# Performance work log

Measured on AMD Instinct MI355X. Metric: run time of the kernel, lower is better.

The kernel has to match this reference:

```python
import jax, jax.numpy as jnp
import numpy as np

N_AGENTS, HIDDEN, MSG, KEY = 8192, 256, 128, 64

def _glorot(k, shape):
    fan_in, fan_out = shape[0], shape[1]
    lim = jnp.sqrt(6.0 / (fan_in + fan_out))
    return jax.random.uniform(k, shape, jnp.float32, -lim, lim)

def setup_inputs() -> dict:
    key = jax.random.key(0)
    ks = jax.random.split(key, 12)
    inp = {
        'h': jax.random.normal(ks[0], (N_AGENTS, HIDDEN), jnp.float32),
        'W_msg': _glorot(ks[1], (HIDDEN, MSG)), 'b_msg': jnp.zeros((MSG,), jnp.float32),
        'W_key': _glorot(ks[2], (HIDDEN, KEY)), 'b_key': jnp.zeros((KEY,), jnp.float32),
        'W_qry': _glorot(ks[3], (HIDDEN, KEY)), 'b_qry': jnp.zeros((KEY,), jnp.float32),
        # GRUCell: input (attended message, dim MSG) -> hidden; gates r,z,n
        'Wi_r': _glorot(ks[4], (MSG, HIDDEN)), 'bi_r': jnp.zeros((HIDDEN,), jnp.float32),
        'Wi_z': _glorot(ks[5], (MSG, HIDDEN)), 'bi_z': jnp.zeros((HIDDEN,), jnp.float32),
        'Wi_n': _glorot(ks[6], (MSG, HIDDEN)), 'bi_n': jnp.zeros((HIDDEN,), jnp.float32),
        'Wh_r': _glorot(ks[7], (HIDDEN, HIDDEN)),
        'Wh_z': _glorot(ks[8], (HIDDEN, HIDDEN)),
        'Wh_n': _glorot(ks[9], (HIDDEN, HIDDEN)), 'bh_n': jnp.zeros((HIDDEN,), jnp.float32),
    }
    return inp

def reference(h, W_msg, b_msg, W_key, b_key, W_qry, b_qry,
              Wi_r, bi_r, Wi_z, bi_z, Wi_n, bi_n, Wh_r, Wh_z, Wh_n, bh_n):
    n = h.shape[0]
    messages = h @ W_msg + b_msg            # [N, MSG]
    keys = h @ W_key + b_key                # [N, KEY]
    queries = h @ W_qry + b_qry             # [N, KEY]
    scale = jnp.sqrt(jnp.float32(keys.shape[-1]))
    scores = (queries @ keys.T) / scale     # [N, N]
    scores = jnp.clip(scores, -20.0, 20.0)
    self_mask = jnp.eye(n, dtype=scores.dtype)
    scores = jnp.where(self_mask > 0, -1e8, scores)
    attn_weights = jax.nn.softmax(scores, axis=-1)
    attended = attn_weights @ messages      # [N, MSG]
    # flax GRUCell: carry = h, inputs = attended
    r = jax.nn.sigmoid(attended @ Wi_r + bi_r + h @ Wh_r)
    z = jax.nn.sigmoid(attended @ Wi_z + bi_z + h @ Wh_z)
    cand = jnp.tanh(attended @ Wi_n + bi_n + r * (h @ Wh_n + bh_n))
    h_new = (1.0 - z) * cand + z * h
    return (h_new, attn_weights)
```

## Files before the change

### kernel.cpp

```cpp
#include <hip/hip_runtime.h>
#include <math.h>

#define N_AGENTS 8192
#define HIDDEN   256
#define MSG      128
#define KEYD     64
#define CSPLIT   4

#define OFF_WM_H   0
#define OFF_WM_L   32768
#define OFF_WK_H   65536
#define OFF_WK_L   81920
#define OFF_WQ_H   98304
#define OFF_WQ_L   114688
#define OFF_WIR_H  131072
#define OFF_WIR_L  163840
#define OFF_WIZ_H  196608
#define OFF_WIZ_L  229376
#define OFF_WIN_H  262144
#define OFF_WIN_L  294912
#define OFF_WHR_H  327680
#define OFF_WHR_L  393216
#define OFF_WHZ_H  458752
#define OFF_WHZ_L  524288
#define OFF_WHN_H  589824
#define OFF_WHN_L  655360
#define WT_TOTAL   720896

typedef __attribute__((ext_vector_type(8))) short short8_t;
typedef __attribute__((ext_vector_type(4))) short short4_t;
typedef __attribute__((ext_vector_type(4))) float float4_t;

__device__ __forceinline__ short f2bf(float x) {
    unsigned u = __float_as_uint(x);
    unsigned r = (u + 0x7fffu + ((u >> 16) & 1u)) >> 16;
    return (short)r;
}
__device__ __forceinline__ float bf2f(short b) {
    return __uint_as_float(((unsigned)(unsigned short)b) << 16);
}
__device__ __forceinline__ void split4(float4 v, short4_t* hi, short4_t* lo) {
    (*hi)[0] = f2bf(v.x); (*lo)[0] = f2bf(v.x - bf2f((*hi)[0]));
    (*hi)[1] = f2bf(v.y); (*lo)[1] = f2bf(v.y - bf2f((*hi)[1]));
    (*hi)[2] = f2bf(v.z); (*lo)[2] = f2bf(v.z - bf2f((*hi)[2]));
    (*hi)[3] = f2bf(v.w); (*lo)[3] = f2bf(v.w - bf2f((*hi)[3]));
}

__global__ __launch_bounds__(256) void prep_weights(
    const float* __restrict__ Wm, const float* __restrict__ Wk, const float* __restrict__ Wq,
    const float* __restrict__ Wir, const float* __restrict__ Wiz, const float* __restrict__ Win,
    const float* __restrict__ Whr, const float* __restrict__ Whz, const float* __restrict__ Whn,
    short* __restrict__ wT)
{
    int idx = blockIdx.x * 256 + threadIdx.x;
    const float* src; int K, lgC, local; size_t oh, ol;
    if (idx < 32768)        { src = Wm;  K = 256; lgC = 7; local = idx;          oh = OFF_WM_H;  ol = OFF_WM_L; }
    else if (idx < 49152)   { src = Wk;  K = 256; lgC = 6; local = idx - 32768;  oh = OFF_WK_H;  ol = OFF_WK_L; }
    else if (idx < 65536)   { src = Wq;  K = 256; lgC = 6; local = idx - 49152;  oh = OFF_WQ_H;  ol = OFF_WQ_L; }
    else if (idx < 98304)   { src = Wir; K = 128; lgC = 8; local = idx - 65536;  oh = OFF_WIR_H; ol = OFF_WIR_L; }
    else if (idx < 131072)  { src = Wiz; K = 128; lgC = 8; local = idx - 98304;  oh = OFF_WIZ_H; ol = OFF_WIZ_L; }
    else if (idx < 163840)  { src = Win; K = 128; lgC = 8; local = idx - 131072; oh = OFF_WIN_H; ol = OFF_WIN_L; }
    else if (idx < 229376)  { src = Whr; K = 256; lgC = 8; local = idx - 163840; oh = OFF_WHR_H; ol = OFF_WHR_L; }
    else if (idx < 294912)  { src = Whz; K = 256; lgC = 8; local = idx - 229376; oh = OFF_WHZ_H; ol = OFF_WHZ_L; }
    else if (idx < 360448)  { src = Whn; K = 256; lgC = 8; local = idx - 294912; oh = OFF_WHN_H; ol = OFF_WHN_L; }
    else return;
    int k = local >> lgC, c = local & ((1 << lgC) - 1);
    float v = src[local];
    short hi = f2bf(v);
    short lo = f2bf(v - bf2f(hi));
    wT[oh + (size_t)c * K + k] = hi;
    wT[ol + (size_t)c * K + k] = lo;
}

__global__ __launch_bounds__(256) void proj_mfma_kernel(
    const float* __restrict__ h, const short* __restrict__ wT,
    const float* __restrict__ bm, const float* __restrict__ bk, const float* __restrict__ bq,
    short* __restrict__ msgTb,
    short* __restrict__ qh, short* __restrict__ ql,
    short* __restrict__ kh, short* __restrict__ kl)
{
    __shared__ short hh[16][264], hl[16][264];
    int t = threadIdx.x;
    int wave = t >> 6, l = t & 63, quad = l >> 4, ln = l & 15;
    int i0 = blockIdx.x * 16;

#pragma unroll
    for (int p = 0; p < 4; p++) {
        int idx = t + p * 256;
        int r = idx >> 6, k4 = (idx & 63) * 4;
        float4 v = *(const float4*)&h[(size_t)(i0 + r) * HIDDEN + k4];
        short4_t hv, lv;
        split4(v, &hv, &lv);
        *(short4_t*)&hh[r][k4] = hv;
        *(short4_t*)&hl[r][k4] = lv;
    }
    __syncthreads();

    size_t base_h, base_l; int cb;
    if (wave < 2)      { base_h = OFF_WM_H; base_l = OFF_WM_L; cb = wave * 64; }
    else if (wave == 2){ base_h = OFF_WK_H; base_l = OFF_WK_L; cb = 0; }
    else               { base_h = OFF_WQ_H; base_l = OFF_WQ_L; cb = 0; }

    float4_t acc[4];
#pragma unroll
    for (int nt = 0; nt < 4; nt++) acc[nt] = (float4_t)0.f;

    for (int ch = 0; ch < 8; ch++) {
        short8_t a_h = *(short8_t*)&hh[ln][ch * 32 + quad * 8];
        short8_t a_l = *(short8_t*)&hl[ln][ch * 32 + quad * 8];
#pragma unroll
        for (int nt = 0; nt < 4; nt++) {
            int c = cb + nt * 16 + ln;
            const short* bp_h = wT + base_h + (size_t)c * 256 + ch * 32 + quad * 8;
            const short* bp_l = wT + base_l + (size_t)c * 256 + ch * 32 + quad * 8;
            short8_t b_h = *(const short8_t*)bp_h;
            short8_t b_l = *(const short8_t*)bp_l;
            acc[nt] = __builtin_amdgcn_mfma_f32_16x16x32_bf16(a_h, b_h, acc[nt], 0, 0, 0);
            acc[nt] = __builtin_amdgcn_mfma_f32_16x16x32_bf16(a_h, b_l, acc[nt], 0, 0, 0);
            acc[nt] = __builtin_amdgcn_mfma_f32_16x16x32_bf16(a_l, b_h, acc[nt], 0, 0, 0);
        }
    }

    if (wave < 2) {
#pragma unroll
        for (int nt = 0; nt < 4; nt++) {
            int col = cb + nt * 16 + ln;
            float b = bm[col];
            short4_t o;
#pragma unroll
            for (int reg = 0; reg < 4; reg++) o[reg] = f2bf(acc[nt][reg] + b);
            *(short4_t*)&msgTb[(size_t)col * N_AGENTS + i0 + quad * 4] = o;
        }
    } else {
        short* dh = (wave == 2) ? kh : qh;
        short* dl = (wave == 2) ? kl : ql;
        const float* bias = (wave == 2) ? bk : bq;
#pragma unroll
        for (int nt = 0; nt < 4; nt++) {
            int col = nt * 16 + ln;
            float b = bias[col];
#pragma unroll
            for (int reg = 0; reg < 4; reg++) {
                int row = i0 + quad * 4 + reg;
                float v = acc[nt][reg] + b;
                short hi = f2bf(v);
                short lo = f2bf(v - bf2f(hi));
                dh[(size_t)row * KEYD + col] = hi;
                dl[(size_t)row * KEYD + col] = lo;
            }
        }
    }
}

__global__ __launch_bounds__(256) void rowsum_kernel(
    const short* __restrict__ qh, const short* __restrict__ ql,
    const short* __restrict__ kh, const short* __restrict__ kl,
    float* __restrict__ rowsum)
{
    int t = threadIdx.x;
    int wave = t >> 6, l = t & 63;
    int quad = l >> 4, ln = l & 15;
    int i0 = blockIdx.y * 64;
    int j0 = blockIdx.x * 256 + wave * 64;

    short8_t ah[4][2], al[4][2];
#pragma unroll
    for (int r = 0; r < 4; r++)
#pragma unroll
        for (int ch = 0; ch < 2; ch++) {
            size_t off = (size_t)(i0 + r * 16 + ln) * KEYD + ch * 32 + quad * 8;
            ah[r][ch] = *(const short8_t*)(qh + off);
            al[r][ch] = *(const short8_t*)(ql + off);
        }

    float4_t acc[4][4];
#pragma unroll
    for (int r = 0; r < 4; r++)
#pragma unroll
        for (int c = 0; c < 4; c++) acc[r][c] = (float4_t)0.f;

#pragma unroll
    for (int c = 0; c < 4; c++) {
        int coln = j0 + c * 16 + ln;
#pragma unroll
        for (int ch = 0; ch < 2; ch++) {
            size_t off = (size_t)coln * KEYD + ch * 32 + quad * 8;
            short8_t bh = *(const short8_t*)(kh + off);
            short8_t bl = *(const short8_t*)(kl + off);
#pragma unroll
            for (int r = 0; r < 4; r++) {
                acc[r][c] = __builtin_amdgcn_mfma_f32_16x16x32_bf16(ah[r][ch], bh, acc[r][c], 0, 0, 0);
                acc[r][c] = __builtin_amdgcn_mfma_f32_16x16x32_bf16(ah[r][ch], bl, acc[r][c], 0, 0, 0);
                acc[r][c] = __builtin_amdgcn_mfma_f32_16x16x32_bf16(al[r][ch], bh, acc[r][c], 0, 0, 0);
            }
        }
    }

    float prow[4][4];
#pragma unroll
    for (int r = 0; r < 4; r++)
#pragma unroll
        for (int reg = 0; reg < 4; reg++) {
            int gi = i0 + r * 16 + quad * 4 + reg;
            float sum = 0.f;
#pragma unroll
            for (int c = 0; c < 4; c++) {
                float s = acc[r][c][reg] * 0.125f;
                s = fminf(fmaxf(s, -20.f), 20.f);
                int gj = j0 + c * 16 + ln;
                float p = (gi == gj) ? 0.f : __expf(s);
                sum += p;
            }
            prow[r][reg] = sum;
        }

#pragma unroll
    for (int off = 1; off < 16; off <<= 1)
#pragma unroll
        for (int r = 0; r < 4; r++)
#pragma unroll
            for (int reg = 0; reg < 4; reg++)
                prow[r][reg] += __shfl_xor(prow[r][reg], off);

    if (ln == 0) {
#pragma unroll
        for (int r = 0; r < 4; r++)
#pragma unroll
            for (int reg = 0; reg < 4; reg++)
                atomicAdd(&rowsum[i0 + r * 16 + quad * 4 + reg], prow[r][reg]);
    }
}

__global__ __launch_bounds__(256) void attend_fused_kernel(
    const short* __restrict__ qh, const short* __restrict__ ql,
    const short* __restrict__ kh, const short* __restrict__ kl,
    const short* __restrict__ msgTb, const float* __restrict__ rowsum,
    float* __restrict__ P, float* __restrict__ att_part)
{
    const int JB = 128;
    const int STR = JB + 8;
    __shared__ short A_lds[64][STR];
    __shared__ short B_lds[MSG][STR];
    __shared__ float inv_s[64];

    int t = threadIdx.x;
    int wave = t >> 6, l = t & 63;
    int quad = l >> 4, ln = l & 15;
    int i0 = blockIdx.y * 64;
    int kbase = blockIdx.x * (N_AGENTS / CSPLIT);

    if (t < 64) inv_s[t] = 1.0f / rowsum[i0 + t];

    short8_t ah[4][2], al[4][2];
#pragma unroll
    for (int r = 0; r < 4; r++)
#pragma unroll
        for (int ch = 0; ch < 2; ch++) {
            size_t off = (size_t)(i0 + r * 16 + ln) * KEYD + ch * 32 + quad * 8;
            ah[r][ch] = *(const short8_t*)(qh + off);
            al[r][ch] = *(const short8_t*)(ql + off);
        }

    float4_t accm[8];
#pragma unroll
    for (int c = 0; c < 8; c++) accm[c] = (float4_t)0.f;

    __syncthreads();

    for (int jt = 0; jt < N_AGENTS / CSPLIT; jt += JB) {
        int kpos = kbase + jt;

        float4_t acc[4][2];
#pragma unroll
        for (int r = 0; r < 4; r++)
#pragma unroll
            for (int c2 = 0; c2 < 2; c2++) acc[r][c2] = (float4_t)0.f;

#pragma unroll
        for (int c2 = 0; c2 < 2; c2++) {
            int coln = kpos + wave * 32 + c2 * 16 + ln;
#pragma unroll
            for (int ch = 0; ch < 2; ch++) {
                size_t off = (size_t)coln * KEYD + ch * 32 + quad * 8;
                short8_t bh = *(const short8_t*)(kh + off);
                short8_t bl = *(const short8_t*)(kl + off);
#pragma unroll
                for (int r = 0; r < 4; r++) {
                    acc[r][c2] = __builtin_amdgcn_mfma_f32_16x16x32_bf16(ah[r][ch], bh, acc[r][c2], 0, 0, 0);
                    acc[r][c2] = __builtin_amdgcn_mfma_f32_16x16x32_bf16(ah[r][ch], bl, acc[r][c2], 0, 0, 0);
                    acc[r][c2] = __builtin_amdgcn_mfma_f32_16x16x32_bf16(al[r][ch], bh, acc[r][c2], 0, 0, 0);
                }
            }
        }

        __syncthreads();

        short8_t bst[8];
#pragma unroll
        for (int p = 0; p < 8; p++) {
            int idx = t + p * 256;
            int c = idx >> 4, kk = (idx & 15) * 8;
            bst[p] = *(const short8_t*)(msgTb + (size_t)c * N_AGENTS + kpos + kk);
        }

        float pv[4][4][2];
#pragma unroll
        for (int r = 0; r < 4; r++)
#pragma unroll
            for (int reg = 0; reg < 4; reg++) {
                int row = r * 16 + quad * 4 + reg;
                int gi = i0 + row;
                float iv = inv_s[row];
#pragma unroll
                for (int c2 = 0; c2 < 2; c2++) {
                    int col = wave * 32 + c2 * 16 + ln;
                    int gj = kpos + col;
                    float s = acc[r][c2][reg] * 0.125f;
                    s = fminf(fmaxf(s, -20.f), 20.f);
                    float p = (gi == gj) ? 0.f : __expf(s) * iv;
                    pv[r][reg][c2] = p;
                    A_lds[row][col] = f2bf(p);
                }
            }

#pragma unroll
        for (int p = 0; p < 8; p++) {
            int idx = t + p * 256;
            int c = idx >> 4, kk = (idx & 15) * 8;
            *(short8_t*)&B_lds[c][kk] = bst[p];
        }

        __syncthreads();

#pragma unroll
        for (int r = 0; r < 4; r++)
#pragma unroll
            for (int reg = 0; reg < 4; reg++) {
                int gi = i0 + r * 16 + quad * 4 + reg;
#pragma unroll
                for (int c2 = 0; c2 < 2; c2++) {
                    int gj = kpos + wave * 32 + c2 * 16 + ln;
                    __builtin_nontemporal_store(pv[r][reg][c2], &P[(size_t)gi * N_AGENTS + gj]);
                }
            }

#pragma unroll
        for (int kc = 0; kc < 4; kc++) {
            short8_t a = *(short8_t*)&A_lds[wave * 16 + ln][kc * 32 + quad * 8];
#pragma unroll
            for (int c = 0; c < 8; c++) {
                short8_t b = *(short8_t*)&B_lds[c * 16 + ln][kc * 32 + quad * 8];
                accm[c] = __builtin_amdgcn_mfma_f32_16x16x32_bf16(a, b, accm[c], 0, 0, 0);
            }
        }
    }

    float* ap = att_part + (size_t)blockIdx.x * N_AGENTS * MSG;
#pragma unroll
    for (int c = 0; c < 8; c++)
#pragma unroll
        for (int reg = 0; reg < 4; reg++) {
            int row = i0 + wave * 16 + quad * 4 + reg;
            int col = c * 16 + ln;
            ap[(size_t)row * MSG + col] = accm[c][reg];
        }
}

__global__ __launch_bounds__(256) void gru_mfma_kernel(
    const float* __restrict__ att_part, const float* __restrict__ h,
    const short* __restrict__ wT,
    const float* __restrict__ bir, const float* __restrict__ biz,
    const float* __restrict__ bin, const float* __restrict__ bhn,
    float* __restrict__ hnew)
{
    __shared__ short ath[16][136], atl[16][136];
    __shared__ short hh[16][264], hl[16][264];
    int t = threadIdx.x;
    int wave = t >> 6, l = t & 63, quad = l >> 4, ln = l & 15;
    int i0 = blockIdx.x * 16;
    int cb = wave * 64;

#pragma unroll
    for (int p = 0; p < 2; p++) {
        int idx = t + p * 256;
        int r = idx >> 5, c4 = (idx & 31) * 4;
        size_t off = (size_t)(i0 + r) * MSG + c4;
        float4 v = *(const float4*)&att_part[off];
#pragma unroll
        for (int s = 1; s < CSPLIT; s++) {
            float4 w = *(const float4*)&att_part[(size_t)s * N_AGENTS * MSG + off];
            v.x += w.x; v.y += w.y; v.z += w.z; v.w += w.w;
        }
        short4_t hv, lv;
        split4(v, &hv, &lv);
        *(short4_t*)&ath[r][c4] = hv;
        *(short4_t*)&atl[r][c4] = lv;
    }
#pragma unroll
    for (int p = 0; p < 4; p++) {
        int idx = t + p * 256;
        int r = idx >> 6, k4 = (idx & 63) * 4;
        float4 v = *(const float4*)&h[(size_t)(i0 + r) * HIDDEN + k4];
        short4_t hv, lv;
        split4(v, &hv, &lv);
        *(short4_t*)&hh[r][k4] = hv;
        *(short4_t*)&hl[r][k4] = lv;
    }
    __syncthreads();

    float4_t ar[4], az[4], an[4], hn[4];
#pragma unroll
    for (int nt = 0; nt < 4; nt++) {
        ar[nt] = (float4_t)0.f; az[nt] = (float4_t)0.f;
        an[nt] = (float4_t)0.f; hn[nt] = (float4_t)0.f;
    }

#define MFMA3(ACC, AH, AL, BH, BL)                                              \
    ACC = __builtin_amdgcn_mfma_f32_16x16x32_bf16(AH, BH, ACC, 0, 0, 0);        \
    ACC = __builtin_amdgcn_mfma_f32_16x16x32_bf16(AH, BL, ACC, 0, 0, 0);        \
    ACC = __builtin_amdgcn_mfma_f32_16x16x32_bf16(AL, BH, ACC, 0, 0, 0);

    for (int ch = 0; ch < 4; ch++) {
        short8_t a_h = *(short8_t*)&ath[ln][ch * 32 + quad * 8];
        short8_t a_l = *(short8_t*)&atl[ln][ch * 32 + quad * 8];
#pragma unroll
        for (int nt = 0; nt < 4; nt++) {
            size_t cw = (size_t)(cb + nt * 16 + ln) * 128 + ch * 32 + quad * 8;
            short8_t brh = *(const short8_t*)(wT + OFF_WIR_H + cw);
            short8_t brl = *(const short8_t*)(wT + OFF_WIR_L + cw);
            MFMA3(ar[nt], a_h, a_l, brh, brl);
            short8_t bzh = *(const short8_t*)(wT + OFF_WIZ_H + cw);
            short8_t bzl = *(const short8_t*)(wT + OFF_WIZ_L + cw);
            MFMA3(az[nt], a_h, a_l, bzh, bzl);
            short8_t bnh = *(const short8_t*)(wT + OFF_WIN_H + cw);
            short8_t bnl = *(const short8_t*)(wT + OFF_WIN_L + cw);
            MFMA3(an[nt], a_h, a_l, bnh, bnl);
        }
    }

    for (int ch = 0; ch < 8; ch++) {
        short8_t a_h = *(short8_t*)&hh[ln][ch * 32 + quad * 8];
        short8_t a_l = *(short8_t*)&hl[ln][ch * 32 + quad * 8];
#pragma unroll
        for (int nt = 0; nt < 4; nt++) {
            size_t cw = (size_t)(cb + nt * 16 + ln) * 256 + ch * 32 + quad * 8;
            short8_t brh = *(const short8_t*)(wT + OFF_WHR_H + cw);
            short8_t brl = *(const short8_t*)(wT + OFF_WHR_L + cw);
            MFMA3(ar[nt], a_h, a_l, brh, brl);
            short8_t bzh = *(const short8_t*)(wT + OFF_WHZ_H + cw);
            short8_t bzl = *(const short8_t*)(wT + OFF_WHZ_L + cw);
            MFMA3(az[nt], a_h, a_l, bzh, bzl);
            short8_t bnh = *(const short8_t*)(wT + OFF_WHN_H + cw);
            short8_t bnl = *(const short8_t*)(wT + OFF_WHN_L + cw);
            MFMA3(hn[nt], a_h, a_l, bnh, bnl);
        }
    }
#undef MFMA3

#pragma unroll
    for (int nt = 0; nt < 4; nt++) {
        int col = cb + nt * 16 + ln;
        float br = bir[col], bz = biz[col], bn = bin[col], bh_ = bhn[col];
#pragma unroll
        for (int reg = 0; reg < 4; reg++) {
            int row = i0 + quad * 4 + reg;
            float hv = h[(size_t)row * HIDDEN + col];
            float rr = 1.f / (1.f + __expf(-(ar[nt][reg] + br)));
            float zz = 1.f / (1.f + __expf(-(az[nt][reg] + bz)));
            float cand = tanhf(an[nt][reg] + bn + rr * (hn[nt][reg] + bh_));
            hnew[(size_t)row * HIDDEN + col] = (1.f - zz) * cand + zz * hv;
        }
    }
}

extern "C" void kernel_launch(void* const* d_in, const int* in_sizes, int n_in,
                              void* d_out, int out_size, void* d_ws, size_t ws_size,
                              hipStream_t stream)
{
    const float* h     = (const float*)d_in[0];
    const float* W_msg = (const float*)d_in[1];
    const float* b_msg = (const float*)d_in[2];
    const float* W_key = (const float*)d_in[3];
    const float* b_key = (const float*)d_in[4];
    const float* W_qry = (const float*)d_in[5];
    const float* b_qry = (const float*)d_in[6];
    const float* Wi_r  = (const float*)d_in[7];
    const float* bi_r  = (const float*)d_in[8];
    const float* Wi_z  = (const float*)d_in[9];
    const float* bi_z  = (const float*)d_in[10];
    const float* Wi_n  = (const float*)d_in[11];
    const float* bi_n  = (const float*)d_in[12];
    const float* Wh_r  = (const float*)d_in[13];
    const float* Wh_z  = (const float*)d_in[14];
    const float* Wh_n  = (const float*)d_in[15];
    const float* bh_n  = (const float*)d_in[16];

    float* out  = (float*)d_out;
    float* hnew = out;
    float* P    = out + (size_t)N_AGENTS * HIDDEN;

    float* ws       = (float*)d_ws;
    float* rowsum   = ws;
    float* att_part = ws + N_AGENTS;
    short* sbase    = (short*)(att_part + (size_t)CSPLIT * N_AGENTS * MSG);
    short* msgTb    = sbase;
    short* qh       = msgTb + (size_t)MSG * N_AGENTS;
    short* ql       = qh + (size_t)N_AGENTS * KEYD;
    short* kh       = ql + (size_t)N_AGENTS * KEYD;
    short* kl       = kh + (size_t)N_AGENTS * KEYD;
    short* wT       = kl + (size_t)N_AGENTS * KEYD;

    hipMemsetAsync(rowsum, 0, (size_t)N_AGENTS * sizeof(float), stream);

    prep_weights<<<1408, 256, 0, stream>>>(W_msg, W_key, W_qry, Wi_r, Wi_z, Wi_n,
                                           Wh_r, Wh_z, Wh_n, wT);

    proj_mfma_kernel<<<N_AGENTS / 16, 256, 0, stream>>>(h, wT, b_msg, b_key, b_qry,
                                                        msgTb, qh, ql, kh, kl);

    rowsum_kernel<<<dim3(N_AGENTS / 256, N_AGENTS / 64), 256, 0, stream>>>(qh, ql, kh, kl, rowsum);

    attend_fused_kernel<<<dim3(CSPLIT, N_AGENTS / 64), 256, 0, stream>>>(qh, ql, kh, kl,
                                                                         msgTb, rowsum, P, att_part);

    gru_mfma_kernel<<<N_AGENTS / 16, 256, 0, stream>>>(att_part, h, wT, bi_r, bi_z, bi_n, bh_n, hnew);
}
```

Measured before the change: 595.8 us.

## Software-pipeline attend kernel with double-buffered LDS and replace rowsum atomics

The attention kernel now processes 64-column key tiles with double-buffered LDS. The next tile's key fragments and message slices are prefetched into registers, and its QK^T MFMAs are issued while the current tile's PV MFMAs run, so a barrier is removed per step. Rowsum atomics and the memset are replaced by per-block partial sums that are reduced in the attend kernel prologue. Launch bounds request 2 blocks per SIMD. These changes add register pressure and a strided partial-sum read.

```diff
diff --git a/kernel.cpp b/kernel.cpp
--- a/kernel.cpp
+++ b/kernel.cpp
@@ -6,6 +6,7 @@
 #define MSG      128
 #define KEYD     64
 #define CSPLIT   4
+#define NSTEP    (N_AGENTS / CSPLIT / 64)
 
 #define OFF_WM_H   0
 #define OFF_WM_L   32768
@@ -111,10 +112,8 @@
 #pragma unroll
         for (int nt = 0; nt < 4; nt++) {
             int c = cb + nt * 16 + ln;
-            const short* bp_h = wT + base_h + (size_t)c * 256 + ch * 32 + quad * 8;
-            const short* bp_l = wT + base_l + (size_t)c * 256 + ch * 32 + quad * 8;
-            short8_t b_h = *(const short8_t*)bp_h;
-            short8_t b_l = *(const short8_t*)bp_l;
+            short8_t b_h = *(const short8_t*)(wT + base_h + (size_t)c * 256 + ch * 32 + quad * 8);
+            short8_t b_l = *(const short8_t*)(wT + base_l + (size_t)c * 256 + ch * 32 + quad * 8);
             acc[nt] = __builtin_amdgcn_mfma_f32_16x16x32_bf16(a_h, b_h, acc[nt], 0, 0, 0);
             acc[nt] = __builtin_amdgcn_mfma_f32_16x16x32_bf16(a_h, b_l, acc[nt], 0, 0, 0);
             acc[nt] = __builtin_amdgcn_mfma_f32_16x16x32_bf16(a_l, b_h, acc[nt], 0, 0, 0);
@@ -155,7 +154,7 @@
 __global__ __launch_bounds__(256) void rowsum_kernel(
     const short* __restrict__ qh, const short* __restrict__ ql,
     const short* __restrict__ kh, const short* __restrict__ kl,
-    float* __restrict__ rowsum)
+    float* __restrict__ rowsum_part)
 {
     int t = threadIdx.x;
     int wave = t >> 6, l = t & 63;
@@ -223,24 +222,23 @@
                 prow[r][reg] += __shfl_xor(prow[r][reg], off);
 
     if (ln == 0) {
+        int pidx = blockIdx.x * 4 + wave;
 #pragma unroll
         for (int r = 0; r < 4; r++)
 #pragma unroll
             for (int reg = 0; reg < 4; reg++)
-                atomicAdd(&rowsum[i0 + r * 16 + quad * 4 + reg], prow[r][reg]);
-    }
-}
-
-__global__ __launch_bounds__(256) void attend_fused_kernel(
+                rowsum_part[(size_t)(i0 + r * 16 + quad * 4 + reg) * 128 + pidx] = prow[r][reg];
+    }
+}
+
+__global__ __launch_bounds__(256, 2) void attend_fused_kernel(
     const short* __restrict__ qh, const short* __restrict__ ql,
     const short* __restrict__ kh, const short* __restrict__ kl,
-    const short* __restrict__ msgTb, const float* __restrict__ rowsum,
+    const short* __restrict__ msgTb, const float* __restrict__ rowsum_part,
     float* __restrict__ P, float* __restrict__ att_part)
 {
-    const int JB = 128;
-    const int STR = JB + 8;
-    __shared__ short A_lds[64][STR];
-    __shared__ short B_lds[MSG][STR];
+    __shared__ short A_lds[2][64][72];
+    __shared__ short B_lds[2][128][72];
     __shared__ float inv_s[64];
 
     int t = threadIdx.x;
@@ -249,7 +247,16 @@
     int i0 = blockIdx.y * 64;
     int kbase = blockIdx.x * (N_AGENTS / CSPLIT);
 
-    if (t < 64) inv_s[t] = 1.0f / rowsum[i0 + t];
+    if (t < 64) {
+        const float* rp = rowsum_part + (size_t)(i0 + t) * 128;
+        float s = 0.f;
+#pragma unroll
+        for (int p = 0; p < 32; p++) {
+            float4 v = *(const float4*)(rp + p * 4);
+            s += v.x + v.y + v.z + v.w;
+        }
+        inv_s[t] = 1.0f / s;
+    }
 
     short8_t ah[4][2], al[4][2];
 #pragma unroll
@@ -265,69 +272,71 @@
 #pragma unroll
     for (int c = 0; c < 8; c++) accm[c] = (float4_t)0.f;
 
+    const int colL = wave * 16 + ln;
+
+    short8_t kfh[2], kfl[2];
+    short8_t bst[4];
+    {
+        int coln = kbase + colL;
+#pragma unroll
+        for (int ch = 0; ch < 2; ch++) {
+            size_t off = (size_t)coln * KEYD + ch * 32 + quad * 8;
+            kfh[ch] = *(const short8_t*)(kh + off);
+            kfl[ch] = *(const short8_t*)(kl + off);
+        }
+#pragma unroll
+        for (int p = 0; p < 4; p++) {
+            int idx = t + p * 256;
+            int c = idx >> 3, kk = (idx & 7) * 8;
+            bst[p] = *(const short8_t*)(msgTb + (size_t)c * N_AGENTS + kbase + kk);
+        }
+    }
+    float4_t acc[4];
+#pragma unroll
+    for (int r = 0; r < 4; r++) acc[r] = (float4_t)0.f;
+#pragma unroll
+    for (int ch = 0; ch < 2; ch++)
+#pragma unroll
+        for (int r = 0; r < 4; r++) {
+            acc[r] = __builtin_amdgcn_mfma_f32_16x16x32_bf16(ah[r][ch], kfh[ch], acc[r], 0, 0, 0);
+            acc[r] = __builtin_amdgcn_mfma_f32_16x16x32_bf16(ah[r][ch], kfl[ch], acc[r], 0, 0, 0);
+            acc[r] = __builtin_amdgcn_mfma_f32_16x16x32_bf16(al[r][ch], kfh[ch], acc[r], 0, 0, 0);
+        }
+
     __syncthreads();
 
-    for (int jt = 0; jt < N_AGENTS / CSPLIT; jt += JB) {
-        int kpos = kbase + jt;
-
-        float4_t acc[4][2];
-#pragma unroll
-        for (int r = 0; r < 4; r++)
-#pragma unroll
-            for (int c2 = 0; c2 < 2; c2++) acc[r][c2] = (float4_t)0.f;
-
-#pragma unroll
-        for (int c2 = 0; c2 < 2; c2++) {
-            int coln = kpos + wave * 32 + c2 * 16 + ln;
-#pragma unroll
-            for (int ch = 0; ch < 2; ch++) {
-                size_t off = (size_t)coln * KEYD + ch * 32 + quad * 8;
-                short8_t bh = *(const short8_t*)(kh + off);
-                short8_t bl = *(const short8_t*)(kl + off);
-#pragma unroll
-                for (int r = 0; r < 4; r++) {
-                    acc[r][c2] = __builtin_amdgcn_mfma_f32_16x16x32_bf16(ah[r][ch], bh, acc[r][c2], 0, 0, 0);
-                    acc[r][c2] = __builtin_amdgcn_mfma_f32_16x16x32_bf16(ah[r][ch], bl, acc[r][c2], 0, 0, 0);
-                    acc[r][c2] = __builtin_amdgcn_mfma_f32_16x16x32_bf16(al[r][ch], bh, acc[r][c2], 0, 0, 0);
-                }
-            }
-        }
-
-        __syncthreads();
-
-        short8_t bst[8];
-#pragma unroll
-        for (int p = 0; p < 8; p++) {
-            int idx = t + p * 256;
-            int c = idx >> 4, kk = (idx & 15) * 8;
-            bst[p] = *(const short8_t*)(msgTb + (size_t)c * N_AGENTS + kpos + kk);
-        }
-
-        float pv[4][4][2];
+    float vinv[4][4];
+#pragma unroll
+    for (int r = 0; r < 4; r++)
+#pragma unroll
+        for (int reg = 0; reg < 4; reg++)
+            vinv[r][reg] = inv_s[r * 16 + quad * 4 + reg];
+
+    float pv[4][4];
+
+    for (int st = 0; st < NSTEP; st++) {
+        int buf = st & 1;
+        int kpos = kbase + st * 64;
+
 #pragma unroll
         for (int r = 0; r < 4; r++)
 #pragma unroll
             for (int reg = 0; reg < 4; reg++) {
                 int row = r * 16 + quad * 4 + reg;
                 int gi = i0 + row;
-                float iv = inv_s[row];
-#pragma unroll
-                for (int c2 = 0; c2 < 2; c2++) {
-                    int col = wave * 32 + c2 * 16 + ln;
-                    int gj = kpos + col;
-                    float s = acc[r][c2][reg] * 0.125f;
-                    s = fminf(fmaxf(s, -20.f), 20.f);
-                    float p = (gi == gj) ? 0.f : __expf(s) * iv;
-                    pv[r][reg][c2] = p;
-                    A_lds[row][col] = f2bf(p);
-                }
-            }
-
-#pragma unroll
-        for (int p = 0; p < 8; p++) {
+                float s = acc[r][reg] * 0.125f;
+                s = fminf(fmaxf(s, -20.f), 20.f);
+                int gj = kpos + colL;
+                float p = (gi == gj) ? 0.f : __expf(s) * vinv[r][reg];
+                pv[r][reg] = p;
+                A_lds[buf][row][colL] = f2bf(p);
+            }
+
+#pragma unroll
+        for (int p = 0; p < 4; p++) {
             int idx = t + p * 256;
-            int c = idx >> 4, kk = (idx & 15) * 8;
-            *(short8_t*)&B_lds[c][kk] = bst[p];
+            int c = idx >> 3, kk = (idx & 7) * 8;
+            *(short8_t*)&B_lds[buf][c][kk] = bst[p];
         }
 
         __syncthreads();
@@ -337,21 +346,47 @@
 #pragma unroll
             for (int reg = 0; reg < 4; reg++) {
                 int gi = i0 + r * 16 + quad * 4 + reg;
-#pragma unroll
-                for (int c2 = 0; c2 < 2; c2++) {
-                    int gj = kpos + wave * 32 + c2 * 16 + ln;
-                    __builtin_nontemporal_store(pv[r][reg][c2], &P[(size_t)gi * N_AGENTS + gj]);
+                __builtin_nontemporal_store(pv[r][reg], &P[(size_t)gi * N_AGENTS + kpos + colL]);
+            }
+
+        if (st + 1 < NSTEP) {
+            int kp2 = kpos + 64;
+            int coln = kp2 + colL;
+#pragma unroll
+            for (int ch = 0; ch < 2; ch++) {
+                size_t off = (size_t)coln * KEYD + ch * 32 + quad * 8;
+                kfh[ch] = *(const short8_t*)(kh + off);
+                kfl[ch] = *(const short8_t*)(kl + off);
+            }
+#pragma unroll
+            for (int p = 0; p < 4; p++) {
+                int idx = t + p * 256;
+                int c = idx >> 3, kk = (idx & 7) * 8;
+                bst[p] = *(const short8_t*)(msgTb + (size_t)c * N_AGENTS + kp2 + kk);
+            }
+        }
+
+#pragma unroll
+        for (int kc = 0; kc < 2; kc++) {
+            short8_t a = *(short8_t*)&A_lds[buf][wave * 16 + ln][kc * 32 + quad * 8];
+#pragma unroll
+            for (int c = 0; c < 8; c++) {
+                short8_t b = *(short8_t*)&B_lds[buf][c * 16 + ln][kc * 32 + quad * 8];
+                accm[c] = __builtin_amdgcn_mfma_f32_16x16x32_bf16(a, b, accm[c], 0, 0, 0);
+            }
+        }
+
+        if (st + 1 < NSTEP) {
+#pragma unroll
+            for (int r = 0; r < 4; r++) acc[r] = (float4_t)0.f;
+#pragma unroll
+            for (int ch = 0; ch < 2; ch++)
+#pragma unroll
+                for (int r = 0; r < 4; r++) {
+                    acc[r] = __builtin_amdgcn_mfma_f32_16x16x32_bf16(ah[r][ch], kfh[ch], acc[r], 0, 0, 0);
+                    acc[r] = __builtin_amdgcn_mfma_f32_16x16x32_bf16(ah[r][ch], kfl[ch], acc[r], 0, 0, 0);
+                    acc[r] = __builtin_amdgcn_mfma_f32_16x16x32_bf16(al[r][ch], kfh[ch], acc[r], 0, 0, 0);
                 }
-            }
-
-#pragma unroll
-        for (int kc = 0; kc < 4; kc++) {
-            short8_t a = *(short8_t*)&A_lds[wave * 16 + ln][kc * 32 + quad * 8];
-#pragma unroll
-            for (int c = 0; c < 8; c++) {
-                short8_t b = *(short8_t*)&B_lds[c * 16 + ln][kc * 32 + quad * 8];
-                accm[c] = __builtin_amdgcn_mfma_f32_16x16x32_bf16(a, b, accm[c], 0, 0, 0);
-            }
         }
     }
 
@@ -499,18 +534,16 @@
     float* hnew = out;
     float* P    = out + (size_t)N_AGENTS * HIDDEN;
 
-    float* ws       = (float*)d_ws;
-    float* rowsum   = ws;
-    float* att_part = ws + N_AGENTS;
-    short* sbase    = (short*)(att_part + (size_t)CSPLIT * N_AGENTS * MSG);
-    short* msgTb    = sbase;
-    short* qh       = msgTb + (size_t)MSG * N_AGENTS;
-    short* ql       = qh + (size_t)N_AGENTS * KEYD;
-    short* kh       = ql + (size_t)N_AGENTS * KEYD;
-    short* kl       = kh + (size_t)N_AGENTS * KEYD;
-    short* wT       = kl + (size_t)N_AGENTS * KEYD;
-
-    hipMemsetAsync(rowsum, 0, (size_t)N_AGENTS * sizeof(float), stream);
+    float* ws          = (float*)d_ws;
+    float* rowsum_part = ws;
+    float* att_part    = ws + (size_t)N_AGENTS * 128;
+    short* sbase       = (short*)(att_part + (size_t)CSPLIT * N_AGENTS * MSG);
+    short* msgTb       = sbase;
+    short* qh          = msgTb + (size_t)MSG * N_AGENTS;
+    short* ql          = qh + (size_t)N_AGENTS * KEYD;
+    short* kh          = ql + (size_t)N_AGENTS * KEYD;
+    short* kl          = kh + (size_t)N_AGENTS * KEYD;
+    short* wT          = kl + (size_t)N_AGENTS * KEYD;
 
     prep_weights<<<1408, 256, 0, stream>>>(W_msg, W_key, W_qry, Wi_r, Wi_z, Wi_n,
                                            Wh_r, Wh_z, Wh_n, wT);
@@ -518,10 +551,12 @@
     proj_mfma_kernel<<<N_AGENTS / 16, 256, 0, stream>>>(h, wT, b_msg, b_key, b_qry,
                                                         msgTb, qh, ql, kh, kl);
 
-    rowsum_kernel<<<dim3(N_AGENTS / 256, N_AGENTS / 64), 256, 0, stream>>>(qh, ql, kh, kl, rowsum);
+    rowsum_kernel<<<dim3(N_AGENTS / 256, N_AGENTS / 64), 256, 0, stream>>>(qh, ql, kh, kl,
+                                                                           rowsum_part);
 
     attend_fused_kernel<<<dim3(CSPLIT, N_AGENTS / 64), 256, 0, stream>>>(qh, ql, kh, kl,
-                                                                         msgTb, rowsum, P, att_part);
+                                                                         msgTb, rowsum_part,
+                                                                         P, att_part);
 
     gru_mfma_kernel<<<N_AGENTS / 16, 256, 0, stream>>>(att_part, h, wT, bi_r, bi_z, bi_n, bh_n, hnew);
 }
```

Result: faster. 528.2 us (-11.3%).
